# Kernel optimization log

Measured on AMD Instinct MI355X. Metric: run time of the kernel, lower is better.

Reference implementation:

```python
import jax, jax.numpy as jnp
import numpy as np

NPOINT = 1024
NSAMPLE = 32


def _fps(xyz, npoint):
    # farthest point sampling; xyz: (B, N, 3) -> idx (B, npoint) int32
    B, N, _ = xyz.shape

    def step(carry, _):
        dist, far = carry
        centroid = jnp.take_along_axis(xyz, far[:, None, None], axis=1)  # (B,1,3)
        d = jnp.sum((xyz - centroid) ** 2, axis=-1)  # (B,N)
        dist = jnp.minimum(dist, d)
        nxt = jnp.argmax(dist, axis=1).astype(jnp.int32)
        return (dist, nxt), far

    init = (jnp.full((B, N), 1e10, xyz.dtype), jnp.zeros((B,), jnp.int32))
    _, idx = jax.lax.scan(step, init, None, length=npoint)
    return idx.T  # (B, npoint)


def _forward(xyz, features, afa_w1, afa_b1, afa_w2, afa_b2, afa_ww, afa_bw,
             mlp_w1, mlp_b1, mlp_w2, mlp_b2, mlp_w3, mlp_b3):
    B, N, _ = xyz.shape
    M = NSAMPLE
    # --- furthest point sampling + gather new_xyz ---
    fps_idx = _fps(xyz, NPOINT)                                   # (B, Np)
    new_xyz = jnp.take_along_axis(xyz, fps_idx[..., None], axis=1)  # (B, Np, 3)
    # --- kNN grouping (QueryAndGroup with use_xyz) ---
    sqd = (jnp.sum(new_xyz ** 2, -1)[..., None]
           + jnp.sum(xyz ** 2, -1)[:, None, :]
           - 2.0 * jnp.einsum('bpd,bnd->bpn', new_xyz, xyz))       # (B, Np, N)
    _, knn = jax.lax.top_k(-sqd, M)                               # (B, Np, M)
    gather = jax.vmap(lambda a, i: a[i])
    gxyz = gather(xyz, knn) - new_xyz[:, :, None, :]              # (B, Np, M, 3)
    gfeat = gather(features.transpose(0, 2, 1), knn)              # (B, Np, M, Cin)
    x = jnp.concatenate([gxyz, gfeat], axis=-1).transpose(0, 3, 1, 2)  # (B, C, Np, M)
    # --- AFA: pairwise diff + eye self term ---
    eye = jnp.eye(M, dtype=x.dtype)
    pair = x[..., :, None] - x[..., None, :] + x[..., :, None] * eye  # (B, C, Np, M, M)
    conv5 = lambda w, b, t: jnp.einsum('oc,bcnij->bonij', w, t) + b[None, :, None, None, None]
    h = jax.nn.relu(conv5(afa_w1, afa_b1, pair))
    h = jax.nn.relu(conv5(afa_w2, afa_b2, h))
    wgt = conv5(afa_ww, afa_bw, h)                                 # (B, C, Np, M, M)
    afa = jnp.sum(pair * wgt, axis=-1)                             # (B, C, Np, M)
    nf = x + afa
    # --- shared MLP (1x1 convs, relu, no bn) + max pool over M ---
    conv4 = lambda w, b, t: jnp.einsum('oc,bcnm->bonm', w, t) + b[None, :, None, None]
    h = jax.nn.relu(conv4(mlp_w1, mlp_b1, nf))
    h = jax.nn.relu(conv4(mlp_w2, mlp_b2, h))
    h = jax.nn.relu(conv4(mlp_w3, mlp_b3, h))
    out = jnp.max(h, axis=-1)                                      # (B, 128, Np)
    return new_xyz, out


def setup_inputs() -> dict:
    key = jax.random.key(0)
    ks = jax.random.split(key, 10)
    B, N, Cin = 2, 4096, 32
    C = Cin + 3  # use_xyz adds 3 -> 35

    def w(k, o, i):
        return (jax.random.normal(k, (o, i), jnp.float32) / np.float32(np.sqrt(i)))

    return {
        'xyz': jax.random.uniform(ks[0], (B, N, 3), jnp.float32),
        'features': jax.random.normal(ks[1], (B, Cin, N), jnp.float32),
        'afa_w1': w(ks[2], 16, C), 'afa_b1': jnp.zeros((16,), jnp.float32),
        'afa_w2': w(ks[3], 16, 16), 'afa_b2': jnp.zeros((16,), jnp.float32),
        'afa_ww': w(ks[4], C, 16), 'afa_bw': jnp.zeros((C,), jnp.float32),
        'mlp_w1': w(ks[5], 64, C), 'mlp_b1': jnp.zeros((64,), jnp.float32),
        'mlp_w2': w(ks[6], 64, 64), 'mlp_b2': jnp.zeros((64,), jnp.float32),
        'mlp_w3': w(ks[7], 128, 64), 'mlp_b3': jnp.zeros((128,), jnp.float32),
    }


def reference(xyz, features, afa_w1, afa_b1, afa_w2, afa_b2, afa_ww, afa_bw,
              mlp_w1, mlp_b1, mlp_w2, mlp_b2, mlp_w3, mlp_b3):
    return _forward(xyz, features, afa_w1, afa_b1, afa_w2, afa_b2, afa_ww, afa_bw,
                    mlp_w1, mlp_b1, mlp_w2, mlp_b2, mlp_w3, mlp_b3)
```

## Files before the change

### kernel.cpp

```cpp
#include <hip/hip_runtime.h>

#define BB 2
#define NN 4096
#define NP 1024
#define MM 32
#define CC 35
#define CIN 32

typedef float f2 __attribute__((ext_vector_type(2)));

#define KEY_DPP(CTRL) do { \
    int _lo = (int)(unsigned)key, _hi = (int)(unsigned)(key >> 32); \
    int _olo = __builtin_amdgcn_mov_dpp(_lo, CTRL, 0xF, 0xF, true); \
    int _ohi = __builtin_amdgcn_mov_dpp(_hi, CTRL, 0xF, 0xF, true); \
    unsigned long long _ok = ((unsigned long long)(unsigned)_ohi << 32) | (unsigned)_olo; \
    if (_ok > key) key = _ok; \
} while (0)

__launch_bounds__(256)
__global__ void fps_prep_kernel(const float* __restrict__ xyz, float* __restrict__ newxyz_out,
                                const float* __restrict__ w1, const float* __restrict__ w2,
                                const float* __restrict__ w3,
                                float* __restrict__ w1T, float* __restrict__ w2T,
                                float* __restrict__ w3T)
{
#pragma clang fp contract(off)
    const int t = threadIdx.x;

    if (blockIdx.x >= BB) {
        int g = (blockIdx.x - BB) * 256 + t;
        int stride = 8 * 256;
        for (int i = g; i < 64 * CC; i += stride) { int o = i / CC, c = i % CC; w1T[c * 64 + o] = w1[i]; }
        for (int i = g; i < 64 * 64; i += stride) { int o = i >> 6, c = i & 63; w2T[c * 64 + o] = w2[i]; }
        for (int i = g; i < 128 * 64; i += stride) { int o = i >> 6, c = i & 63; w3T[c * 128 + o] = w3[i]; }
        return;
    }

    const int b = blockIdx.x;
    const float* xb = xyz + b * NN * 3;

    __shared__ float4 pc[NN];
    __shared__ float nxs[NP * 3];
    __shared__ unsigned long long red[2][16];

    f2 px[8], py[8], pz[8], dist[8];
#pragma unroll
    for (int k = 0; k < 16; ++k) {
        int n = t + 256 * k;
        float x = xb[n * 3 + 0];
        float y = xb[n * 3 + 1];
        float z = xb[n * 3 + 2];
        px[k >> 1][k & 1] = x;
        py[k >> 1][k & 1] = y;
        pz[k >> 1][k & 1] = z;
        dist[k >> 1][k & 1] = 1e10f;
        pc[n] = make_float4(x, y, z, 0.0f);
    }
    __syncthreads();

    int far = 0;
    for (int s = 0; s < NP; ++s) {
        float4 c = pc[far];
        if (t == 0) {
            nxs[s * 3 + 0] = c.x;
            nxs[s * 3 + 1] = c.y;
            nxs[s * 3 + 2] = c.z;
        }
        const f2 cx = { c.x, c.x }, cy = { c.y, c.y }, cz = { c.z, c.z };

        float bv = -1.0f; int bi = 0;
#pragma unroll
        for (int j = 0; j < 8; ++j) {
            f2 dx = px[j] - cx, dy = py[j] - cy, dz = pz[j] - cz;
            f2 d = (dx * dx + dy * dy) + dz * dz;
            f2 dd = __builtin_elementwise_min(dist[j], d);
            dist[j] = dd;
            if (dd.x > bv) { bv = dd.x; bi = t + 256 * (2 * j); }
            if (dd.y > bv) { bv = dd.y; bi = t + 256 * (2 * j + 1); }
        }

        unsigned long long key =
            ((unsigned long long)(unsigned)__float_as_int(bv) << 32)
            | (unsigned)(0xFFFFFFFFu - (unsigned)bi);

        KEY_DPP(0xB1);
        KEY_DPP(0x4E);
        KEY_DPP(0x141);
        KEY_DPP(0x140);

        const int buf = s & 1;
        if ((t & 15) == 0) red[buf][t >> 4] = key;
        __syncthreads();

        key = red[buf][t & 15];
        KEY_DPP(0xB1);
        KEY_DPP(0x4E);
        KEY_DPP(0x141);
        KEY_DPP(0x140);
        far = (int)(0xFFFFFFFFu - (unsigned)key);
    }

    __syncthreads();
#pragma unroll
    for (int j = 0; j < 12; ++j) {
        int i = t + 256 * j;
        newxyz_out[b * NP * 3 + i] = nxs[i];
    }
}

__launch_bounds__(256)
__global__ void knn_kernel(const float* __restrict__ xyz, const float* __restrict__ newxyz,
                           int* __restrict__ knn_out)
{
#pragma clang fp contract(off)
    const int bp = blockIdx.x;
    const int b = bp >> 10;
    const int t = threadIdx.x;
    const float* xb = xyz + b * NN * 3;

    const float qx = newxyz[bp * 3 + 0];
    const float qy = newxyz[bp * 3 + 1];
    const float qz = newxyz[bp * 3 + 2];
    const float qn = (qx * qx + qy * qy) + qz * qz;

    __shared__ unsigned kxs[NN];
    __shared__ int hist[256];
    __shared__ int wsum[4];
    __shared__ unsigned long long blist[512];
    __shared__ int scal[4];

    hist[t] = 0;
    if (t < 4) scal[t] = 0;
    __syncthreads();

#pragma unroll
    for (int k = 0; k < 16; ++k) {
        int n = t + 256 * k;
        float x = xb[n * 3 + 0], y = xb[n * 3 + 1], z = xb[n * 3 + 2];
        float xn = (x * x + y * y) + z * z;
        float dt = (qx * x + qy * y) + qz * z;
        float d = (qn + xn) - 2.0f * dt;
        unsigned bits = __float_as_uint(d);
        unsigned kx = bits ^ ((unsigned)((int)bits >> 31) | 0x80000000u);
        kxs[n] = kx;
        atomicAdd(&hist[kx >> 24], 1);
    }
    __syncthreads();

    {
        int c = hist[t];
        int incl = c;
        const int lane = t & 63, w = t >> 6;
#pragma unroll
        for (int off = 1; off < 64; off <<= 1) {
            int o = __shfl_up(incl, off);
            if (lane >= off) incl += o;
        }
        if (lane == 63) wsum[w] = incl;
        __syncthreads();
        int base = 0;
        for (int ww = 0; ww < 4; ++ww) if (ww < w) base += wsum[ww];
        int excl = base + incl - c;
        if (excl < MM && MM <= excl + c) { scal[0] = t; scal[1] = excl; }
    }
    __syncthreads();

    const int B = scal[0];
    const int cntBelow = scal[1];
    const unsigned bstart = (unsigned)B << 24;

#pragma unroll
    for (int k = 0; k < 16; ++k) {
        int n = t + 256 * k;
        unsigned kx = kxs[n];
        if (kx < bstart) {
            int pos = atomicAdd(&scal[3], 1);
            knn_out[bp * MM + pos] = n;
        } else if ((kx >> 24) == (unsigned)B) {
            int pos = atomicAdd(&scal[2], 1);
            if (pos < 512) blist[pos] = ((unsigned long long)kx << 32) | (unsigned)n;
        }
    }
    __syncthreads();

    const int nB = scal[2];
    const int k2 = MM - cntBelow;

    if (nB <= 512) {
        for (int m = t; m < nB; m += 256) {
            unsigned long long my = blist[m];
            int rank = 0;
            for (int q = 0; q < nB; ++q) rank += (blist[q] < my) ? 1 : 0;
            if (rank < k2)
                knn_out[bp * MM + (cntBelow + rank)] = (int)(my & 0xFFFFFFFFu);
        }
    } else {
        for (int r = 0; r < MM; ++r) {
            unsigned bvk = 0xFFFFFFFFu; int bi = NN;
#pragma unroll
            for (int k = 0; k < 16; ++k) {
                int n = t + 256 * k;
                unsigned v = kxs[n];
                if (v < bvk) { bvk = v; bi = n; }
            }
#pragma unroll
            for (int off = 1; off < 64; off <<= 1) {
                unsigned ov = __shfl_xor(bvk, off);
                int   oi = __shfl_xor(bi, off);
                if (ov < bvk || (ov == bvk && oi < bi)) { bvk = ov; bi = oi; }
            }
            if ((t & 63) == 0) { hist[t >> 6] = (int)bvk; wsum[t >> 6] = bi; }
            __syncthreads();
            unsigned fv = (unsigned)hist[0]; int fi = wsum[0];
#pragma unroll
            for (int w = 1; w < 4; ++w) {
                unsigned ov = (unsigned)hist[w]; int oi = wsum[w];
                if (ov < fv || (ov == fv && oi < fi)) { fv = ov; fi = oi; }
            }
            if (t == 0) { knn_out[bp * MM + r] = fi; kxs[fi] = 0xFFFFFFFFu; }
            __syncthreads();
        }
    }
}

__launch_bounds__(256)
__global__ void afa_mlp_kernel(const float* __restrict__ xyz, const float* __restrict__ feat,
                               const float* __restrict__ newxyz, const int* __restrict__ knn,
                               const float* __restrict__ aw1, const float* __restrict__ ab1,
                               const float* __restrict__ aw2, const float* __restrict__ ab2,
                               const float* __restrict__ aww, const float* __restrict__ abw,
                               const float* __restrict__ w1T, const float* __restrict__ b1,
                               const float* __restrict__ w2T, const float* __restrict__ b2,
                               const float* __restrict__ w3T, const float* __restrict__ b3,
                               float* __restrict__ out)
{
    const int bp = blockIdx.x;
    const int b = bp >> 10, p = bp & 1023;
    const int t = threadIdx.x;

    __shared__ int   idxs[MM];
    __shared__ float xs_t[MM][36];
    __shared__ float u_lds[MM][20];
    __shared__ float nfs[CC][MM];
    __shared__ float h1s[64][36];
    __shared__ float h2s[64][36];
    __shared__ float pmax[128][2];

    if (t < MM) idxs[t] = knn[bp * MM + t];
    __syncthreads();

    {
        const int m = t & 31, c0 = t >> 5;
        const int id = idxs[m] & (NN - 1);
        for (int c = c0; c < CC; c += 8) {
            float v;
            if (c < 3) v = xyz[(b * NN + id) * 3 + c] - newxyz[bp * 3 + c];
            else       v = feat[(b * CIN + (c - 3)) * NN + id];
            xs_t[m][c] = v;
        }
        if (c0 == 0) xs_t[m][35] = 0.0f;
    }
    __syncthreads();

    const int i = t >> 3, jg = t & 7;

    float xi[36];
    {
        const float4* xp = (const float4*)&xs_t[i][0];
#pragma unroll
        for (int q = 0; q < 9; ++q) {
            float4 v = xp[q];
            xi[4 * q] = v.x; xi[4 * q + 1] = v.y; xi[4 * q + 2] = v.z; xi[4 * q + 3] = v.w;
        }
    }

    float u16[16];
#pragma unroll
    for (int o = 0; o < 16; ++o) {
        float acc = 0.0f;
#pragma unroll
        for (int c = 0; c < CC; ++c) acc += aw1[o * CC + c] * xi[c];
        u16[o] = acc;
    }
    if (jg == 0) {
        float4* up = (float4*)&u_lds[i][0];
#pragma unroll
        for (int q = 0; q < 4; ++q)
            up[q] = make_float4(u16[4 * q], u16[4 * q + 1], u16[4 * q + 2], u16[4 * q + 3]);
    }
    __syncthreads();

    float afa[CC];
#pragma unroll
    for (int c = 0; c < CC; ++c) afa[c] = 0.0f;

#pragma unroll
    for (int jk = 0; jk < 4; ++jk) {
        const int j = jg + 8 * jk;
        const bool diag = (i == j);

        float uj[16];
        {
            const float4* up = (const float4*)&u_lds[j][0];
#pragma unroll
            for (int q = 0; q < 4; ++q) {
                float4 v = up[q];
                uj[4 * q] = v.x; uj[4 * q + 1] = v.y; uj[4 * q + 2] = v.z; uj[4 * q + 3] = v.w;
            }
        }

        float h1[16];
#pragma unroll
        for (int o = 0; o < 16; ++o) {
            float sv = u16[o] - uj[o];
            if (diag) sv += u16[o];
            h1[o] = fmaxf(sv + ab1[o], 0.0f);
        }

        float xj[36];
        {
            const float4* xp = (const float4*)&xs_t[j][0];
#pragma unroll
            for (int q = 0; q < 9; ++q) {
                float4 v = xp[q];
                xj[4 * q] = v.x; xj[4 * q + 1] = v.y; xj[4 * q + 2] = v.z; xj[4 * q + 3] = v.w;
            }
        }

        float h2[16];
#pragma unroll
        for (int o = 0; o < 16; ++o) {
            float acc = ab2[o];
#pragma unroll
            for (int c = 0; c < 16; ++c) acc += aw2[o * 16 + c] * h1[c];
            h2[o] = fmaxf(acc, 0.0f);
        }

#pragma unroll
        for (int c = 0; c < CC; ++c) {
            float acc = abw[c];
#pragma unroll
            for (int k = 0; k < 16; ++k) acc += aww[c * 16 + k] * h2[k];
            float pc_ = xi[c] - xj[c];
            if (diag) pc_ += xi[c];
            afa[c] += pc_ * acc;
        }
    }

#pragma unroll
    for (int c = 0; c < CC; ++c) {
        float v = afa[c];
        v += __shfl_xor(v, 1);
        v += __shfl_xor(v, 2);
        v += __shfl_xor(v, 4);
        if (jg == 0) nfs[c][i] = xi[c] + v;
    }
    __syncthreads();

    {
        const int o = t & 63, ib = (t >> 6) << 3;
        float acc[8];
        float bb = b1[o];
#pragma unroll
        for (int k = 0; k < 8; ++k) acc[k] = bb;
        for (int c = 0; c < CC; ++c) {
            float w = w1T[c * 64 + o];
            const float4* np4 = (const float4*)&nfs[c][ib];
            float4 n0 = np4[0], n1 = np4[1];
            acc[0] += w * n0.x; acc[1] += w * n0.y; acc[2] += w * n0.z; acc[3] += w * n0.w;
            acc[4] += w * n1.x; acc[5] += w * n1.y; acc[6] += w * n1.z; acc[7] += w * n1.w;
        }
        float4 r0 = { fmaxf(acc[0], 0.0f), fmaxf(acc[1], 0.0f), fmaxf(acc[2], 0.0f), fmaxf(acc[3], 0.0f) };
        float4 r1 = { fmaxf(acc[4], 0.0f), fmaxf(acc[5], 0.0f), fmaxf(acc[6], 0.0f), fmaxf(acc[7], 0.0f) };
        *(float4*)&h1s[o][ib]     = r0;
        *(float4*)&h1s[o][ib + 4] = r1;
    }
    __syncthreads();

    {
        const int o = t & 63, ib = (t >> 6) << 3;
        float acc[8];
        float bb = b2[o];
#pragma unroll
        for (int k = 0; k < 8; ++k) acc[k] = bb;
        for (int c = 0; c < 64; ++c) {
            float w = w2T[c * 64 + o];
            const float4* hp4 = (const float4*)&h1s[c][ib];
            float4 h0 = hp4[0], h1v = hp4[1];
            acc[0] += w * h0.x; acc[1] += w * h0.y; acc[2] += w * h0.z; acc[3] += w * h0.w;
            acc[4] += w * h1v.x; acc[5] += w * h1v.y; acc[6] += w * h1v.z; acc[7] += w * h1v.w;
        }
        float4 r0 = { fmaxf(acc[0], 0.0f), fmaxf(acc[1], 0.0f), fmaxf(acc[2], 0.0f), fmaxf(acc[3], 0.0f) };
        float4 r1 = { fmaxf(acc[4], 0.0f), fmaxf(acc[5], 0.0f), fmaxf(acc[6], 0.0f), fmaxf(acc[7], 0.0f) };
        *(float4*)&h2s[o][ib]     = r0;
        *(float4*)&h2s[o][ib + 4] = r1;
    }
    __syncthreads();

    {
        const int o = t & 127, ib = (t >> 7) << 4;
        float acc[16];
        float bb = b3[o];
#pragma unroll
        for (int k = 0; k < 16; ++k) acc[k] = bb;
        for (int c = 0; c < 64; ++c) {
            float w = w3T[c * 128 + o];
            const float4* hp4 = (const float4*)&h2s[c][ib];
            float4 h0 = hp4[0], h1v = hp4[1], h2v = hp4[2], h3v = hp4[3];
            acc[0]  += w * h0.x;  acc[1]  += w * h0.y;  acc[2]  += w * h0.z;  acc[3]  += w * h0.w;
            acc[4]  += w * h1v.x; acc[5]  += w * h1v.y; acc[6]  += w * h1v.z; acc[7]  += w * h1v.w;
            acc[8]  += w * h2v.x; acc[9]  += w * h2v.y; acc[10] += w * h2v.z; acc[11] += w * h2v.w;
            acc[12] += w * h3v.x; acc[13] += w * h3v.y; acc[14] += w * h3v.z; acc[15] += w * h3v.w;
        }
        float mx = -1e30f;
#pragma unroll
        for (int k = 0; k < 16; ++k) mx = fmaxf(mx, fmaxf(acc[k], 0.0f));
        pmax[o][t >> 7] = mx;
    }
    __syncthreads();

    if (t < 128) {
        float v = fmaxf(pmax[t][0], pmax[t][1]);
        out[(b * 128 + t) * NP + p] = v;
    }
}

extern "C" void kernel_launch(void* const* d_in, const int* in_sizes, int n_in,
                              void* d_out, int out_size, void* d_ws, size_t ws_size,
                              hipStream_t stream)
{
    const float* xyz  = (const float*)d_in[0];
    const float* feat = (const float*)d_in[1];
    const float* aw1  = (const float*)d_in[2];
    const float* ab1  = (const float*)d_in[3];
    const float* aw2  = (const float*)d_in[4];
    const float* ab2  = (const float*)d_in[5];
    const float* aww  = (const float*)d_in[6];
    const float* abw  = (const float*)d_in[7];
    const float* mw1  = (const float*)d_in[8];
    const float* mb1  = (const float*)d_in[9];
    const float* mw2  = (const float*)d_in[10];
    const float* mb2  = (const float*)d_in[11];
    const float* mw3  = (const float*)d_in[12];
    const float* mb3  = (const float*)d_in[13];

    float* out    = (float*)d_out;
    float* newxyz = out;
    float* out2   = out + BB * NP * 3;

    int*   knn = (int*)d_ws;
    float* w1T = (float*)((char*)d_ws + (1 << 19));
    float* w2T = w1T + CC * 64;
    float* w3T = w2T + 64 * 64;

    fps_prep_kernel<<<dim3(BB + 8), dim3(256), 0, stream>>>(xyz, newxyz,
                                                            mw1, mw2, mw3, w1T, w2T, w3T);
    knn_kernel<<<dim3(BB * NP), dim3(256), 0, stream>>>(xyz, newxyz, knn);
    afa_mlp_kernel<<<dim3(BB * NP), dim3(256), 0, stream>>>(
        xyz, feat, newxyz, knn,
        aw1, ab1, aw2, ab2, aww, abw,
        w1T, mb1, w2T, mb2, w3T, mb3, out2);
}
```

Baseline: 719.0 us.

## Fuse kNN selection into AFA/MLP kernel and pack MLP weights as float4

Merges the kNN kernel into the AFA+MLP kernel so neighbour indices stay in shared memory instead of round-tripping through global memory. The two kernels' shared buffers are overlaid with a union. It removes one launch and the global write/read of the knn indices. MLP weights are repacked into groups of four input channels so each thread loads a float4 per four channels. The AFA first-layer projection is now split across thread groups, two outputs each, instead of every thread computing all 16. In exchange the fused kernel may have higher register pressure and more shared memory, which could lower occupancy.

```diff
diff --git a/kernel.cpp b/kernel.cpp
--- a/kernel.cpp
+++ b/kernel.cpp
@@ -21,8 +21,8 @@
 __global__ void fps_prep_kernel(const float* __restrict__ xyz, float* __restrict__ newxyz_out,
                                 const float* __restrict__ w1, const float* __restrict__ w2,
                                 const float* __restrict__ w3,
-                                float* __restrict__ w1T, float* __restrict__ w2T,
-                                float* __restrict__ w3T)
+                                float* __restrict__ w1p, float* __restrict__ w2p,
+                                float* __restrict__ w3p)
 {
 #pragma clang fp contract(off)
     const int t = threadIdx.x;
@@ -30,9 +30,19 @@
     if (blockIdx.x >= BB) {
         int g = (blockIdx.x - BB) * 256 + t;
         int stride = 8 * 256;
-        for (int i = g; i < 64 * CC; i += stride) { int o = i / CC, c = i % CC; w1T[c * 64 + o] = w1[i]; }
-        for (int i = g; i < 64 * 64; i += stride) { int o = i >> 6, c = i & 63; w2T[c * 64 + o] = w2[i]; }
-        for (int i = g; i < 128 * 64; i += stride) { int o = i >> 6, c = i & 63; w3T[c * 128 + o] = w3[i]; }
+        for (int i = g; i < 9 * 64 * 4; i += stride) {
+            int c4 = i >> 8, o = (i >> 2) & 63, cl = i & 3;
+            int c = 4 * c4 + cl;
+            w1p[i] = (c < CC) ? w1[o * CC + c] : 0.0f;
+        }
+        for (int i = g; i < 16 * 64 * 4; i += stride) {
+            int c4 = i >> 8, o = (i >> 2) & 63, cl = i & 3;
+            w2p[i] = w2[o * 64 + 4 * c4 + cl];
+        }
+        for (int i = g; i < 16 * 128 * 4; i += stride) {
+            int c4 = i >> 9, o = (i >> 2) & 127, cl = i & 3;
+            w3p[i] = w3[o * 64 + 4 * c4 + cl];
+        }
         return;
     }
 
@@ -109,144 +119,141 @@
 }
 
 __launch_bounds__(256)
-__global__ void knn_kernel(const float* __restrict__ xyz, const float* __restrict__ newxyz,
-                           int* __restrict__ knn_out)
-{
-#pragma clang fp contract(off)
-    const int bp = blockIdx.x;
-    const int b = bp >> 10;
-    const int t = threadIdx.x;
-    const float* xb = xyz + b * NN * 3;
-
-    const float qx = newxyz[bp * 3 + 0];
-    const float qy = newxyz[bp * 3 + 1];
-    const float qz = newxyz[bp * 3 + 2];
-    const float qn = (qx * qx + qy * qy) + qz * qz;
-
-    __shared__ unsigned kxs[NN];
-    __shared__ int hist[256];
-    __shared__ int wsum[4];
-    __shared__ unsigned long long blist[512];
-    __shared__ int scal[4];
-
-    hist[t] = 0;
-    if (t < 4) scal[t] = 0;
-    __syncthreads();
-
-#pragma unroll
-    for (int k = 0; k < 16; ++k) {
-        int n = t + 256 * k;
-        float x = xb[n * 3 + 0], y = xb[n * 3 + 1], z = xb[n * 3 + 2];
-        float xn = (x * x + y * y) + z * z;
-        float dt = (qx * x + qy * y) + qz * z;
-        float d = (qn + xn) - 2.0f * dt;
-        unsigned bits = __float_as_uint(d);
-        unsigned kx = bits ^ ((unsigned)((int)bits >> 31) | 0x80000000u);
-        kxs[n] = kx;
-        atomicAdd(&hist[kx >> 24], 1);
-    }
-    __syncthreads();
-
-    {
-        int c = hist[t];
-        int incl = c;
-        const int lane = t & 63, w = t >> 6;
-#pragma unroll
-        for (int off = 1; off < 64; off <<= 1) {
-            int o = __shfl_up(incl, off);
-            if (lane >= off) incl += o;
-        }
-        if (lane == 63) wsum[w] = incl;
-        __syncthreads();
-        int base = 0;
-        for (int ww = 0; ww < 4; ++ww) if (ww < w) base += wsum[ww];
-        int excl = base + incl - c;
-        if (excl < MM && MM <= excl + c) { scal[0] = t; scal[1] = excl; }
-    }
-    __syncthreads();
-
-    const int B = scal[0];
-    const int cntBelow = scal[1];
-    const unsigned bstart = (unsigned)B << 24;
-
-#pragma unroll
-    for (int k = 0; k < 16; ++k) {
-        int n = t + 256 * k;
-        unsigned kx = kxs[n];
-        if (kx < bstart) {
-            int pos = atomicAdd(&scal[3], 1);
-            knn_out[bp * MM + pos] = n;
-        } else if ((kx >> 24) == (unsigned)B) {
-            int pos = atomicAdd(&scal[2], 1);
-            if (pos < 512) blist[pos] = ((unsigned long long)kx << 32) | (unsigned)n;
-        }
-    }
-    __syncthreads();
-
-    const int nB = scal[2];
-    const int k2 = MM - cntBelow;
-
-    if (nB <= 512) {
-        for (int m = t; m < nB; m += 256) {
-            unsigned long long my = blist[m];
-            int rank = 0;
-            for (int q = 0; q < nB; ++q) rank += (blist[q] < my) ? 1 : 0;
-            if (rank < k2)
-                knn_out[bp * MM + (cntBelow + rank)] = (int)(my & 0xFFFFFFFFu);
-        }
-    } else {
-        for (int r = 0; r < MM; ++r) {
-            unsigned bvk = 0xFFFFFFFFu; int bi = NN;
-#pragma unroll
-            for (int k = 0; k < 16; ++k) {
-                int n = t + 256 * k;
-                unsigned v = kxs[n];
-                if (v < bvk) { bvk = v; bi = n; }
-            }
-#pragma unroll
-            for (int off = 1; off < 64; off <<= 1) {
-                unsigned ov = __shfl_xor(bvk, off);
-                int   oi = __shfl_xor(bi, off);
-                if (ov < bvk || (ov == bvk && oi < bi)) { bvk = ov; bi = oi; }
-            }
-            if ((t & 63) == 0) { hist[t >> 6] = (int)bvk; wsum[t >> 6] = bi; }
-            __syncthreads();
-            unsigned fv = (unsigned)hist[0]; int fi = wsum[0];
-#pragma unroll
-            for (int w = 1; w < 4; ++w) {
-                unsigned ov = (unsigned)hist[w]; int oi = wsum[w];
-                if (ov < fv || (ov == fv && oi < fi)) { fv = ov; fi = oi; }
-            }
-            if (t == 0) { knn_out[bp * MM + r] = fi; kxs[fi] = 0xFFFFFFFFu; }
-            __syncthreads();
-        }
-    }
-}
-
-__launch_bounds__(256)
-__global__ void afa_mlp_kernel(const float* __restrict__ xyz, const float* __restrict__ feat,
-                               const float* __restrict__ newxyz, const int* __restrict__ knn,
-                               const float* __restrict__ aw1, const float* __restrict__ ab1,
-                               const float* __restrict__ aw2, const float* __restrict__ ab2,
-                               const float* __restrict__ aww, const float* __restrict__ abw,
-                               const float* __restrict__ w1T, const float* __restrict__ b1,
-                               const float* __restrict__ w2T, const float* __restrict__ b2,
-                               const float* __restrict__ w3T, const float* __restrict__ b3,
-                               float* __restrict__ out)
+__global__ void knnafa_kernel(const float* __restrict__ xyz, const float* __restrict__ feat,
+                              const float* __restrict__ newxyz,
+                              const float* __restrict__ aw1, const float* __restrict__ ab1,
+                              const float* __restrict__ aw2, const float* __restrict__ ab2,
+                              const float* __restrict__ aww, const float* __restrict__ abw,
+                              const float* __restrict__ w1p, const float* __restrict__ b1,
+                              const float* __restrict__ w2p, const float* __restrict__ b2,
+                              const float* __restrict__ w3p, const float* __restrict__ b3,
+                              float* __restrict__ out)
 {
     const int bp = blockIdx.x;
     const int b = bp >> 10, p = bp & 1023;
     const int t = threadIdx.x;
 
-    __shared__ int   idxs[MM];
-    __shared__ float xs_t[MM][36];
-    __shared__ float u_lds[MM][20];
-    __shared__ float nfs[CC][MM];
-    __shared__ float h1s[64][36];
-    __shared__ float h2s[64][36];
-    __shared__ float pmax[128][2];
-
-    if (t < MM) idxs[t] = knn[bp * MM + t];
+    union Smem {
+        struct {
+            unsigned kxs[NN];
+            int hist[256];
+            int wsum[4];
+            unsigned long long blist[512];
+        } k;
+        struct {
+            float xs_t[MM][36];
+            float u[MM][20];
+            float nfs[CC + 1][MM];
+            float h1s[64][36];
+            float h2s[64][36];
+            float pmax[128][2];
+        } a;
+    };
+    __shared__ Smem S;
+    __shared__ int idxs[MM];
+    __shared__ int scal[4];
+
+    {
+#pragma clang fp contract(off)
+        const float* xb = xyz + b * NN * 3;
+        const float qx = newxyz[bp * 3 + 0];
+        const float qy = newxyz[bp * 3 + 1];
+        const float qz = newxyz[bp * 3 + 2];
+        const float qn = (qx * qx + qy * qy) + qz * qz;
+
+        S.k.hist[t] = 0;
+        if (t < 4) scal[t] = 0;
+        __syncthreads();
+
+#pragma unroll
+        for (int k = 0; k < 16; ++k) {
+            int n = t + 256 * k;
+            float x = xb[n * 3 + 0], y = xb[n * 3 + 1], z = xb[n * 3 + 2];
+            float xn = (x * x + y * y) + z * z;
+            float dt = (qx * x + qy * y) + qz * z;
+            float d = (qn + xn) - 2.0f * dt;
+            unsigned bits = __float_as_uint(d);
+            unsigned kx = bits ^ ((unsigned)((int)bits >> 31) | 0x80000000u);
+            S.k.kxs[n] = kx;
+            atomicAdd(&S.k.hist[kx >> 24], 1);
+        }
+        __syncthreads();
+
+        {
+            int c = S.k.hist[t];
+            int incl = c;
+            const int lane = t & 63, w = t >> 6;
+#pragma unroll
+            for (int off = 1; off < 64; off <<= 1) {
+                int o = __shfl_up(incl, off);
+                if (lane >= off) incl += o;
+            }
+            if (lane == 63) S.k.wsum[w] = incl;
+            __syncthreads();
+            int base = 0;
+            for (int ww = 0; ww < 4; ++ww) if (ww < w) base += S.k.wsum[ww];
+            int excl = base + incl - c;
+            if (excl < MM && MM <= excl + c) { scal[0] = t; scal[1] = excl; }
+        }
+        __syncthreads();
+
+        const int B = scal[0];
+        const int cntBelow = scal[1];
+        const unsigned bstart = (unsigned)B << 24;
+
+#pragma unroll
+        for (int k = 0; k < 16; ++k) {
+            int n = t + 256 * k;
+            unsigned kx = S.k.kxs[n];
+            if (kx < bstart) {
+                int pos = atomicAdd(&scal[3], 1);
+                idxs[pos] = n;
+            } else if ((kx >> 24) == (unsigned)B) {
+                int pos = atomicAdd(&scal[2], 1);
+                if (pos < 512) S.k.blist[pos] = ((unsigned long long)kx << 32) | (unsigned)n;
+            }
+        }
+        __syncthreads();
+
+        const int nB = scal[2];
+        const int k2 = MM - cntBelow;
+
+        if (nB <= 512) {
+            for (int m = t; m < nB; m += 256) {
+                unsigned long long my = S.k.blist[m];
+                int rank = 0;
+                for (int q = 0; q < nB; ++q) rank += (S.k.blist[q] < my) ? 1 : 0;
+                if (rank < k2)
+                    idxs[cntBelow + rank] = (int)(my & 0xFFFFFFFFu);
+            }
+        } else {
+            for (int r = 0; r < MM; ++r) {
+                unsigned bvk = 0xFFFFFFFFu; int bi = NN;
+#pragma unroll
+                for (int k = 0; k < 16; ++k) {
+                    int n = t + 256 * k;
+                    unsigned v = S.k.kxs[n];
+                    if (v < bvk) { bvk = v; bi = n; }
+                }
+#pragma unroll
+                for (int off = 1; off < 64; off <<= 1) {
+                    unsigned ov = __shfl_xor(bvk, off);
+                    int   oi = __shfl_xor(bi, off);
+                    if (ov < bvk || (ov == bvk && oi < bi)) { bvk = ov; bi = oi; }
+                }
+                if ((t & 63) == 0) { S.k.hist[t >> 6] = (int)bvk; S.k.wsum[t >> 6] = bi; }
+                __syncthreads();
+                unsigned fv = (unsigned)S.k.hist[0]; int fi = S.k.wsum[0];
+#pragma unroll
+                for (int w = 1; w < 4; ++w) {
+                    unsigned ov = (unsigned)S.k.hist[w]; int oi = S.k.wsum[w];
+                    if (ov < fv || (ov == fv && oi < fi)) { fv = ov; fi = oi; }
+                }
+                if (t == 0) { idxs[r] = fi; S.k.kxs[fi] = 0xFFFFFFFFu; }
+                __syncthreads();
+            }
+        }
+    }
     __syncthreads();
 
     {
@@ -256,9 +263,9 @@
             float v;
             if (c < 3) v = xyz[(b * NN + id) * 3 + c] - newxyz[bp * 3 + c];
             else       v = feat[(b * CIN + (c - 3)) * NN + id];
-            xs_t[m][c] = v;
-        }
-        if (c0 == 0) xs_t[m][35] = 0.0f;
+            S.a.xs_t[m][c] = v;
+        }
+        if (c0 == 0) S.a.xs_t[m][35] = 0.0f;
     }
     __syncthreads();
 
@@ -266,7 +273,7 @@
 
     float xi[36];
     {
-        const float4* xp = (const float4*)&xs_t[i][0];
+        const float4* xp = (const float4*)&S.a.xs_t[i][0];
 #pragma unroll
         for (int q = 0; q < 9; ++q) {
             float4 v = xp[q];
@@ -274,21 +281,25 @@
         }
     }
 
-    float u16[16];
-#pragma unroll
-    for (int o = 0; o < 16; ++o) {
+#pragma unroll
+    for (int oo = 0; oo < 2; ++oo) {
+        const int o = 2 * jg + oo;
         float acc = 0.0f;
 #pragma unroll
         for (int c = 0; c < CC; ++c) acc += aw1[o * CC + c] * xi[c];
-        u16[o] = acc;
-    }
-    if (jg == 0) {
-        float4* up = (float4*)&u_lds[i][0];
-#pragma unroll
-        for (int q = 0; q < 4; ++q)
-            up[q] = make_float4(u16[4 * q], u16[4 * q + 1], u16[4 * q + 2], u16[4 * q + 3]);
-    }
-    __syncthreads();
+        S.a.u[i][o] = acc;
+    }
+    __syncthreads();
+
+    float ui[16];
+    {
+        const float4* up = (const float4*)&S.a.u[i][0];
+#pragma unroll
+        for (int q = 0; q < 4; ++q) {
+            float4 v = up[q];
+            ui[4 * q] = v.x; ui[4 * q + 1] = v.y; ui[4 * q + 2] = v.z; ui[4 * q + 3] = v.w;
+        }
+    }
 
     float afa[CC];
 #pragma unroll
@@ -301,7 +312,7 @@
 
         float uj[16];
         {
-            const float4* up = (const float4*)&u_lds[j][0];
+            const float4* up = (const float4*)&S.a.u[j][0];
 #pragma unroll
             for (int q = 0; q < 4; ++q) {
                 float4 v = up[q];
@@ -312,14 +323,14 @@
         float h1[16];
 #pragma unroll
         for (int o = 0; o < 16; ++o) {
-            float sv = u16[o] - uj[o];
-            if (diag) sv += u16[o];
+            float sv = ui[o] - uj[o];
+            if (diag) sv += ui[o];
             h1[o] = fmaxf(sv + ab1[o], 0.0f);
         }
 
         float xj[36];
         {
-            const float4* xp = (const float4*)&xs_t[j][0];
+            const float4* xp = (const float4*)&S.a.xs_t[j][0];
 #pragma unroll
             for (int q = 0; q < 9; ++q) {
                 float4 v = xp[q];
@@ -353,8 +364,9 @@
         v += __shfl_xor(v, 1);
         v += __shfl_xor(v, 2);
         v += __shfl_xor(v, 4);
-        if (jg == 0) nfs[c][i] = xi[c] + v;
-    }
+        if (jg == 0) S.a.nfs[c][i] = xi[c] + v;
+    }
+    if (jg == 0) S.a.nfs[35][i] = 0.0f;
     __syncthreads();
 
     {
@@ -363,17 +375,24 @@
         float bb = b1[o];
 #pragma unroll
         for (int k = 0; k < 8; ++k) acc[k] = bb;
-        for (int c = 0; c < CC; ++c) {
-            float w = w1T[c * 64 + o];
-            const float4* np4 = (const float4*)&nfs[c][ib];
-            float4 n0 = np4[0], n1 = np4[1];
-            acc[0] += w * n0.x; acc[1] += w * n0.y; acc[2] += w * n0.z; acc[3] += w * n0.w;
-            acc[4] += w * n1.x; acc[5] += w * n1.y; acc[6] += w * n1.z; acc[7] += w * n1.w;
+        const float4* wp = (const float4*)w1p;
+#pragma unroll
+        for (int c4 = 0; c4 < 9; ++c4) {
+            float4 w = wp[c4 * 64 + o];
+#pragma unroll
+            for (int cl = 0; cl < 4; ++cl) {
+                const int c = 4 * c4 + cl;
+                float wc = ((const float*)&w)[cl];
+                const float4* np4 = (const float4*)&S.a.nfs[c][ib];
+                float4 n0 = np4[0], n1 = np4[1];
+                acc[0] += wc * n0.x; acc[1] += wc * n0.y; acc[2] += wc * n0.z; acc[3] += wc * n0.w;
+                acc[4] += wc * n1.x; acc[5] += wc * n1.y; acc[6] += wc * n1.z; acc[7] += wc * n1.w;
+            }
         }
         float4 r0 = { fmaxf(acc[0], 0.0f), fmaxf(acc[1], 0.0f), fmaxf(acc[2], 0.0f), fmaxf(acc[3], 0.0f) };
         float4 r1 = { fmaxf(acc[4], 0.0f), fmaxf(acc[5], 0.0f), fmaxf(acc[6], 0.0f), fmaxf(acc[7], 0.0f) };
-        *(float4*)&h1s[o][ib]     = r0;
-        *(float4*)&h1s[o][ib + 4] = r1;
+        *(float4*)&S.a.h1s[o][ib]     = r0;
+        *(float4*)&S.a.h1s[o][ib + 4] = r1;
     }
     __syncthreads();
 
@@ -383,17 +402,24 @@
         float bb = b2[o];
 #pragma unroll
         for (int k = 0; k < 8; ++k) acc[k] = bb;
-        for (int c = 0; c < 64; ++c) {
-            float w = w2T[c * 64 + o];
-            const float4* hp4 = (const float4*)&h1s[c][ib];
-            float4 h0 = hp4[0], h1v = hp4[1];
-            acc[0] += w * h0.x; acc[1] += w * h0.y; acc[2] += w * h0.z; acc[3] += w * h0.w;
-            acc[4] += w * h1v.x; acc[5] += w * h1v.y; acc[6] += w * h1v.z; acc[7] += w * h1v.w;
+        const float4* wp = (const float4*)w2p;
+#pragma unroll
+        for (int c4 = 0; c4 < 16; ++c4) {
+            float4 w = wp[c4 * 64 + o];
+#pragma unroll
+            for (int cl = 0; cl < 4; ++cl) {
+                const int c = 4 * c4 + cl;
+                float wc = ((const float*)&w)[cl];
+                const float4* hp4 = (const float4*)&S.a.h1s[c][ib];
+                float4 h0 = hp4[0], h1v = hp4[1];
+                acc[0] += wc * h0.x; acc[1] += wc * h0.y; acc[2] += wc * h0.z; acc[3] += wc * h0.w;
+                acc[4] += wc * h1v.x; acc[5] += wc * h1v.y; acc[6] += wc * h1v.z; acc[7] += wc * h1v.w;
+            }
         }
         float4 r0 = { fmaxf(acc[0], 0.0f), fmaxf(acc[1], 0.0f), fmaxf(acc[2], 0.0f), fmaxf(acc[3], 0.0f) };
         float4 r1 = { fmaxf(acc[4], 0.0f), fmaxf(acc[5], 0.0f), fmaxf(acc[6], 0.0f), fmaxf(acc[7], 0.0f) };
-        *(float4*)&h2s[o][ib]     = r0;
-        *(float4*)&h2s[o][ib + 4] = r1;
+        *(float4*)&S.a.h2s[o][ib]     = r0;
+        *(float4*)&S.a.h2s[o][ib + 4] = r1;
     }
     __syncthreads();
 
@@ -403,24 +429,31 @@
         float bb = b3[o];
 #pragma unroll
         for (int k = 0; k < 16; ++k) acc[k] = bb;
-        for (int c = 0; c < 64; ++c) {
-            float w = w3T[c * 128 + o];
-            const float4* hp4 = (const float4*)&h2s[c][ib];
-            float4 h0 = hp4[0], h1v = hp4[1], h2v = hp4[2], h3v = hp4[3];
-            acc[0]  += w * h0.x;  acc[1]  += w * h0.y;  acc[2]  += w * h0.z;  acc[3]  += w * h0.w;
-            acc[4]  += w * h1v.x; acc[5]  += w * h1v.y; acc[6]  += w * h1v.z; acc[7]  += w * h1v.w;
-            acc[8]  += w * h2v.x; acc[9]  += w * h2v.y; acc[10] += w * h2v.z; acc[11] += w * h2v.w;
-            acc[12] += w * h3v.x; acc[13] += w * h3v.y; acc[14] += w * h3v.z; acc[15] += w * h3v.w;
+        const float4* wp = (const float4*)w3p;
+#pragma unroll
+        for (int c4 = 0; c4 < 16; ++c4) {
+            float4 w = wp[c4 * 128 + o];
+#pragma unroll
+            for (int cl = 0; cl < 4; ++cl) {
+                const int c = 4 * c4 + cl;
+                float wc = ((const float*)&w)[cl];
+                const float4* hp4 = (const float4*)&S.a.h2s[c][ib];
+                float4 h0 = hp4[0], h1v = hp4[1], h2v = hp4[2], h3v = hp4[3];
+                acc[0]  += wc * h0.x;  acc[1]  += wc * h0.y;  acc[2]  += wc * h0.z;  acc[3]  += wc * h0.w;
+                acc[4]  += wc * h1v.x; acc[5]  += wc * h1v.y; acc[6]  += wc * h1v.z; acc[7]  += wc * h1v.w;
+                acc[8]  += wc * h2v.x; acc[9]  += wc * h2v.y; acc[10] += wc * h2v.z; acc[11] += wc * h2v.w;
+                acc[12] += wc * h3v.x; acc[13] += wc * h3v.y; acc[14] += wc * h3v.z; acc[15] += wc * h3v.w;
+            }
         }
         float mx = -1e30f;
 #pragma unroll
         for (int k = 0; k < 16; ++k) mx = fmaxf(mx, fmaxf(acc[k], 0.0f));
-        pmax[o][t >> 7] = mx;
+        S.a.pmax[o][t >> 7] = mx;
     }
     __syncthreads();
 
     if (t < 128) {
-        float v = fmaxf(pmax[t][0], pmax[t][1]);
+        float v = fmaxf(S.a.pmax[t][0], S.a.pmax[t][1]);
         out[(b * 128 + t) * NP + p] = v;
     }
 }
@@ -448,16 +481,14 @@
     float* newxyz = out;
     float* out2   = out + BB * NP * 3;
 
-    int*   knn = (int*)d_ws;
-    float* w1T = (float*)((char*)d_ws + (1 << 19));
-    float* w2T = w1T + CC * 64;
-    float* w3T = w2T + 64 * 64;
+    float* w1p = (float*)d_ws;
+    float* w2p = w1p + 9 * 64 * 4;
+    float* w3p = w2p + 16 * 64 * 4;
 
     fps_prep_kernel<<<dim3(BB + 8), dim3(256), 0, stream>>>(xyz, newxyz,
-                                                            mw1, mw2, mw3, w1T, w2T, w3T);
-    knn_kernel<<<dim3(BB * NP), dim3(256), 0, stream>>>(xyz, newxyz, knn);
-    afa_mlp_kernel<<<dim3(BB * NP), dim3(256), 0, stream>>>(
-        xyz, feat, newxyz, knn,
+                                                            mw1, mw2, mw3, w1p, w2p, w3p);
+    knnafa_kernel<<<dim3(BB * NP), dim3(256), 0, stream>>>(
+        xyz, feat, newxyz,
         aw1, ab1, aw2, ab2, aww, abw,
-        w1T, mb1, w2T, mb2, w3T, mb3, out2);
+        w1p, mb1, w2p, mb2, w3p, mb3, out2);
 }
```

Result: no change. 715.6 us (-0.5%).
